# Kernel optimization log

Measured on AMD Instinct MI355X. Metric: run time of the kernel, lower is better.

The kernel has to match this reference:

```python
import jax, jax.numpy as jnp
import numpy as np

B, T, J, C, H = 16, 448, 448, 1024, 16
HD = C // H
NEG_INF = float('-inf')


def _layernorm(x, g, b, eps=1e-5):
    mu = jnp.mean(x, axis=-1, keepdims=True)
    var = jnp.var(x, axis=-1, keepdims=True)
    return (x - mu) * jax.lax.rsqrt(var + eps) * g + b


def _heads(x):
    # [B, S, C] -> [B, H, S, HD]
    Bv, S, _ = x.shape
    return x.reshape(Bv, S, H, HD).transpose(0, 2, 1, 3)


def _merge(x):
    # [B, H, S, HD] -> [B, S, C]
    Bv, _, S, _ = x.shape
    return x.transpose(0, 2, 1, 3).reshape(Bv, S, C)


def setup_inputs() -> dict:
    key = jax.random.key(0)
    ks = jax.random.split(key, 16)
    s = 0.02
    return {
        'tgt': jax.random.normal(ks[0], (B, T, C), jnp.float32),
        'src': jax.random.normal(ks[1], (B, J, C), jnp.float32),
        'sa_wqkv': jax.random.normal(ks[2], (C, 3 * C), jnp.float32) * s,
        'sa_wproj': jax.random.normal(ks[3], (C, C), jnp.float32) * s,
        'sa_bproj': jnp.zeros((C,), jnp.float32),
        'ed_wkv': jax.random.normal(ks[4], (C, 2 * C), jnp.float32) * s,
        'ed_wq': jax.random.normal(ks[5], (C, C), jnp.float32) * s,
        'ed_wproj': jax.random.normal(ks[6], (C, C), jnp.float32) * s,
        'ed_bproj': jnp.zeros((C,), jnp.float32),
        'ff_w1': jax.random.normal(ks[7], (C, 4 * C), jnp.float32) * s,
        'ff_b1': jnp.zeros((4 * C,), jnp.float32),
        'ff_w2': jax.random.normal(ks[8], (4 * C, C), jnp.float32) * s,
        'ff_b2': jnp.zeros((C,), jnp.float32),
        'ln1_g': jnp.ones((C,), jnp.float32), 'ln1_b': jnp.zeros((C,), jnp.float32),
        'ln2_g': jnp.ones((C,), jnp.float32), 'ln2_b': jnp.zeros((C,), jnp.float32),
        'ln3_g': jnp.ones((C,), jnp.float32), 'ln3_b': jnp.zeros((C,), jnp.float32),
        'tgt_padding_mask': jnp.zeros((B, T), bool),
    }


def _forward(tgt, src, sa_wqkv, sa_wproj, sa_bproj, ed_wkv, ed_wq, ed_wproj, ed_bproj,
             ff_w1, ff_b1, ff_w2, ff_b2, ln1_g, ln1_b, ln2_g, ln2_b, ln3_g, ln3_b,
             tgt_padding_mask):
    scale = C ** (-0.5)  # NOTE: original scales by full n_embd, not head_size

    # --- masked self-attention on ln1(tgt) ---
    x = _layernorm(tgt, ln1_g, ln1_b)
    qkv = x @ sa_wqkv
    q, k, v = (_heads(t) for t in jnp.split(qkv, 3, axis=-1))
    wei = jnp.einsum('bhtd,bhsd->bhts', q, k) * scale  # [B,H,T,T]
    causal = jnp.tril(jnp.ones((T, T), bool))
    wei = jnp.where(causal[None, None], wei, NEG_INF)
    wei = jnp.where(tgt_padding_mask[:, None, None, :], NEG_INF, wei)
    wei = jax.nn.softmax(wei, axis=-1)
    sa_out = _merge(jnp.einsum('bhts,bhsd->bhtd', wei, v)) @ sa_wproj + sa_bproj
    result = tgt + sa_out

    # --- cross-attention: ln2 applied to BOTH result and src (as in source) ---
    xq = _layernorm(result, ln2_g, ln2_b)
    xs = _layernorm(src, ln2_g, ln2_b)
    kv = xs @ ed_wkv
    k2, v2 = (_heads(t) for t in jnp.split(kv, 2, axis=-1))
    q2 = _heads(xq @ ed_wq)
    wei2 = jnp.einsum('bhtd,bhjd->bhtj', q2, k2) * scale  # [B,H,T,J]
    wei2 = jax.nn.softmax(wei2, axis=-1)
    ed_out = _merge(jnp.einsum('bhtj,bhjd->bhtd', wei2, v2)) @ ed_wproj + ed_bproj
    result = result + ed_out

    # --- FFN on ln3(tgt) (source uses tgt, not result) ---
    h = jax.nn.relu(_layernorm(tgt, ln3_g, ln3_b) @ ff_w1 + ff_b1)
    result = result + (h @ ff_w2 + ff_b2)
    return result


def reference(tgt, src, sa_wqkv, sa_wproj, sa_bproj, ed_wkv, ed_wq, ed_wproj, ed_bproj,
              ff_w1, ff_b1, ff_w2, ff_b2, ln1_g, ln1_b, ln2_g, ln2_b, ln3_g, ln3_b,
              tgt_padding_mask):
    return _forward(tgt, src, sa_wqkv, sa_wproj, sa_bproj, ed_wkv, ed_wq, ed_wproj,
                    ed_bproj, ff_w1, ff_b1, ff_w2, ff_b2, ln1_g, ln1_b, ln2_g, ln2_b,
                    ln3_g, ln3_b, tgt_padding_mask)
```

## Files before the change

kernel.cpp:

```cpp
#include <hip/hip_runtime.h>

typedef __bf16 bf16;
typedef __bf16 bf16x8 __attribute__((ext_vector_type(8)));
typedef float floatx4 __attribute__((ext_vector_type(4)));

__device__ __forceinline__ floatx4 mfma16(bf16x8 a, bf16x8 b, floatx4 c) {
    return __builtin_amdgcn_mfma_f32_16x16x32_bf16(a, b, c, 0, 0, 0);
}

__device__ __forceinline__ void load16_lds(const void* g, void* l) {
    __builtin_amdgcn_global_load_lds(
        (const __attribute__((address_space(1))) void*)g,
        (__attribute__((address_space(3))) void*)(unsigned int)(unsigned long long)l,
        16, 0, 0);
}

__global__ __launch_bounds__(256) void detect_dtype(const bf16* __restrict__ p,
                                                    int* __restrict__ flag) {
    __shared__ int bad;
    if (threadIdx.x == 0) bad = 0;
    __syncthreads();
    int lbad = 0;
    for (int i = threadIdx.x; i < 4096; i += 256) {
        const float v = (float)p[i];
        if (!isfinite(v) || fabsf(v) > 1e10f) lbad = 1;
    }
    if (lbad) atomicOr(&bad, 1);
    __syncthreads();
    if (threadIdx.x == 0) *flag = bad;
}

__global__ __launch_bounds__(256) void convert_vecs(
    const void* bpr, const void* bep, const void* fb1, const void* fb2,
    const void* g1, const void* b1, const void* g2, const void* b2,
    const void* g3, const void* b3, bf16* __restrict__ out,
    const int* __restrict__ flagp) {
    const int fl = *flagp;
    const int idx = blockIdx.x * 256 + threadIdx.x;
    const void* src;
    int off;
    if (idx < 1024)      { src = bpr; off = idx; }
    else if (idx < 2048) { src = bep; off = idx - 1024; }
    else if (idx < 6144) { src = fb1; off = idx - 2048; }
    else if (idx < 7168) { src = fb2; off = idx - 6144; }
    else {
        const void* t[6] = {g1, b1, g2, b2, g3, b3};
        src = t[(idx - 7168) >> 10];
        off = idx & 1023;
    }
    out[idx] = fl ? (bf16)((const float*)src)[off] : ((const bf16*)src)[off];
}

__global__ __launch_bounds__(256) void ln_f32(const float* __restrict__ X,
                                              const bf16* __restrict__ G,
                                              const bf16* __restrict__ Bv,
                                              bf16* __restrict__ Y) {
    const int row = blockIdx.x;
    const int tid = threadIdx.x;
    const float* x = X + (size_t)row * 1024 + tid * 4;
    float v[4];
#pragma unroll
    for (int i = 0; i < 4; i++) v[i] = x[i];
    float s = v[0] + v[1] + v[2] + v[3];
    float q = v[0] * v[0] + v[1] * v[1] + v[2] * v[2] + v[3] * v[3];
#pragma unroll
    for (int off = 32; off >= 1; off >>= 1) {
        s += __shfl_xor(s, off);
        q += __shfl_xor(q, off);
    }
    __shared__ float ss[4], qq[4];
    const int wave = tid >> 6, lane = tid & 63;
    if (lane == 0) { ss[wave] = s; qq[wave] = q; }
    __syncthreads();
    s = ss[0] + ss[1] + ss[2] + ss[3];
    q = qq[0] + qq[1] + qq[2] + qq[3];
    const float mu = s * (1.0f / 1024.0f);
    const float var = q * (1.0f / 1024.0f) - mu * mu;
    const float rs = rsqrtf(var + 1e-5f);
    bf16* y = Y + (size_t)row * 1024 + tid * 4;
    const bf16* g = G + tid * 4;
    const bf16* b = Bv + tid * 4;
#pragma unroll
    for (int i = 0; i < 4; i++)
        y[i] = (bf16)((v[i] - mu) * rs * (float)g[i] + (float)b[i]);
}

__global__ __launch_bounds__(256) void ln_dyn(const void* __restrict__ X,
                                              const bf16* __restrict__ G,
                                              const bf16* __restrict__ Bv,
                                              bf16* __restrict__ Y,
                                              const int* __restrict__ flagp) {
    const int fl = *flagp;
    const int row = blockIdx.x;
    const int tid = threadIdx.x;
    float v[4];
    if (fl) {
        const float* x = (const float*)X + (size_t)row * 1024 + tid * 4;
#pragma unroll
        for (int i = 0; i < 4; i++) v[i] = x[i];
    } else {
        const bf16* x = (const bf16*)X + (size_t)row * 1024 + tid * 4;
#pragma unroll
        for (int i = 0; i < 4; i++) v[i] = (float)x[i];
    }
    float s = v[0] + v[1] + v[2] + v[3];
    float q = v[0] * v[0] + v[1] * v[1] + v[2] * v[2] + v[3] * v[3];
#pragma unroll
    for (int off = 32; off >= 1; off >>= 1) {
        s += __shfl_xor(s, off);
        q += __shfl_xor(q, off);
    }
    __shared__ float ss[4], qq[4];
    const int wave = tid >> 6, lane = tid & 63;
    if (lane == 0) { ss[wave] = s; qq[wave] = q; }
    __syncthreads();
    s = ss[0] + ss[1] + ss[2] + ss[3];
    q = qq[0] + qq[1] + qq[2] + qq[3];
    const float mu = s * (1.0f / 1024.0f);
    const float var = q * (1.0f / 1024.0f) - mu * mu;
    const float rs = rsqrtf(var + 1e-5f);
    bf16* y = Y + (size_t)row * 1024 + tid * 4;
    const bf16* g = G + tid * 4;
    const bf16* b = Bv + tid * 4;
#pragma unroll
    for (int i = 0; i < 4; i++)
        y[i] = (bf16)((v[i] - mu) * rs * (float)g[i] + (float)b[i]);
}

__global__ __launch_bounds__(256) void transpose_all(
    const void* w0, const void* w1, const void* w2, const void* w3,
    const void* w4, const void* w5, const void* w6,
    bf16* __restrict__ out_base, const int* __restrict__ flagp) {
    const int fl = *flagp;
    const int cum[8] = {0, 3072, 4096, 6144, 7168, 8192, 12288, 16384};
    const int ntv[7] = {96, 32, 64, 32, 32, 128, 32};
    const int ldi[7] = {3072, 1024, 2048, 1024, 1024, 4096, 1024};
    const int ldo[7] = {1024, 1024, 1024, 1024, 1024, 1024, 4096};
    const size_t ooff[7] = {0, 3145728, 4194304, 6291456, 7340032, 8388608, 12582912};
    const void* ws[7] = {w0, w1, w2, w3, w4, w5, w6};

    const int g = blockIdx.x;
    int w = 0;
#pragma unroll
    for (int i = 1; i < 7; i++) if (g >= cum[i]) w = i;
    const int t = g - cum[w];
    const int xt = t % ntv[w], yt = t / ntv[w];
    const int n0 = xt * 32, k0 = yt * 32;
    const void* in = ws[w];
    bf16* out = out_base + ooff[w];
    const int ldin = ldi[w], ldout = ldo[w];

    __shared__ bf16 tile[32][33];
    const int x = threadIdx.x, y = threadIdx.y;
#pragma unroll
    for (int i = 0; i < 4; i++) {
        const size_t idx = (size_t)(k0 + y + 8 * i) * ldin + n0 + x;
        tile[y + 8 * i][x] = fl ? (bf16)((const float*)in)[idx]
                                : ((const bf16*)in)[idx];
    }
    __syncthreads();
#pragma unroll
    for (int i = 0; i < 4; i++)
        out[(size_t)(n0 + y + 8 * i) * ldout + k0 + x] = tile[x][y + 8 * i];
}

template <int TN>
__global__ __launch_bounds__(256) void gemm_bt(
    const bf16* __restrict__ A, int lda,
    const bf16* __restrict__ Bt, int ldb,
    const bf16* __restrict__ bias,
    const void* resd,
    const float* resf,
    bf16* outb, float* outf, void* dual,
    const int* __restrict__ flagp,
    int M, int N, int K, int relu) {
    constexpr int NJ = TN / 32;
    __shared__ bf16 As[128 * 64];
    __shared__ bf16 Bs[TN * 64];
    const int fl = *flagp;
    const int tid = threadIdx.x;
    const int wave = tid >> 6, lane = tid & 63;
    const int quad = lane >> 4, l16 = lane & 15;
    const int g = blockIdx.x;
    const int yb = g % 56, xb = g / 56;
    const int m0 = yb * 128, n0 = xb * TN;
    const int wm = (wave >> 1) * 64, wn = (wave & 1) * (TN / 2);

    const int srow = tid >> 3;
    const int sc = (tid & 7) ^ (srow & 7);
    const bf16* gA = A + (size_t)(m0 + srow) * lda + sc * 8;
    const bf16* gB = Bt + (size_t)(n0 + srow) * ldb + sc * 8;

    floatx4 acc[4][NJ] = {};

    for (int k0 = 0; k0 < K; k0 += 64) {
#pragma unroll
        for (int i = 0; i < 4; i++)
            load16_lds(gA + k0 + (size_t)(32 * i) * lda, &As[tid * 8 + i * 2048]);
#pragma unroll
        for (int i = 0; i < TN / 32; i++)
            load16_lds(gB + k0 + (size_t)(32 * i) * ldb, &Bs[tid * 8 + i * 2048]);
        __syncthreads();
        bf16x8 af[4][2], bfr[NJ][2];
#pragma unroll
        for (int i = 0; i < 4; i++)
#pragma unroll
            for (int h = 0; h < 2; h++) {
                const int r = wm + i * 16 + l16;
                const int slot = ((h << 2) + quad) ^ (r & 7);
                af[i][h] = *(const bf16x8*)(&As[r * 64 + slot * 8]);
            }
#pragma unroll
        for (int j = 0; j < NJ; j++)
#pragma unroll
            for (int h = 0; h < 2; h++) {
                const int r = wn + j * 16 + l16;
                const int slot = ((h << 2) + quad) ^ (r & 7);
                bfr[j][h] = *(const bf16x8*)(&Bs[r * 64 + slot * 8]);
            }
#pragma unroll
        for (int i = 0; i < 4; i++)
#pragma unroll
            for (int j = 0; j < NJ; j++) {
                acc[i][j] = mfma16(af[i][0], bfr[j][0], acc[i][j]);
                acc[i][j] = mfma16(af[i][1], bfr[j][1], acc[i][j]);
            }
        __syncthreads();
    }

#pragma unroll
    for (int i = 0; i < 4; i++) {
        const int mbase = m0 + wm + i * 16 + quad * 4;
#pragma unroll
        for (int j = 0; j < NJ; j++) {
            const int n = n0 + wn + j * 16 + l16;
            const float bv = bias ? (float)bias[n] : 0.0f;
#pragma unroll
            for (int r = 0; r < 4; r++) {
                const size_t idx = (size_t)(mbase + r) * N + n;
                float v = acc[i][j][r] + bv;
                if (relu && v < 0.0f) v = 0.0f;
                if (resd) v += fl ? ((const float*)resd)[idx]
                                  : (float)((const bf16*)resd)[idx];
                if (resf) v += resf[idx];
                if (dual) {
                    if (fl) ((float*)dual)[idx] = v;
                    else ((bf16*)dual)[idx] = (bf16)v;
                } else if (outf) {
                    outf[idx] = v;
                } else {
                    outb[idx] = (bf16)v;
                }
            }
        }
    }
}

__global__ __launch_bounds__(256) void attn_kernel(
    const bf16* __restrict__ Q, int qstride,
    const bf16* __restrict__ Kp, int kstride,
    const bf16* __restrict__ Vp, int vstride,
    bf16* __restrict__ O, int causal) {
    const int T_ = 448, HD = 64, OC = 1024;
    const float scale = 0.03125f;
    const int bh = blockIdx.y, b = bh >> 4, h = bh & 15;
    const int q0 = blockIdx.x * 32;
    const int tid = threadIdx.x, wave = tid >> 6, lane = tid & 63;
    const int quad = lane >> 4, l16 = lane & 15;

    __shared__ bf16 Pb[32][464];
    __shared__ bf16 VT[64][40];
    __shared__ float redp[32][4];
    __shared__ float Mbuf[32], Lbuf[32];

    const bf16* qb = Q + (size_t)(b * T_ + q0) * qstride + h * HD;
    const bf16* kb = Kp + (size_t)(b * T_) * kstride + h * HD;
    const bf16* vb = Vp + (size_t)(b * T_) * vstride + h * HD;

    bf16x8 qf[2][2];
#pragma unroll
    for (int qi = 0; qi < 2; qi++)
#pragma unroll
        for (int kh = 0; kh < 2; kh++)
            qf[qi][kh] = *(const bf16x8*)(qb + (size_t)(qi * 16 + l16) * qstride + kh * 32 + quad * 8);

    float S[2][7][4];
#pragma unroll
    for (int kt = 0; kt < 7; kt++) {
        const int s = wave * 112 + kt * 16 + l16;
        const bf16* kr = kb + (size_t)s * kstride + quad * 8;
        bf16x8 kf0 = *(const bf16x8*)kr;
        bf16x8 kf1 = *(const bf16x8*)(kr + 32);
#pragma unroll
        for (int qi = 0; qi < 2; qi++) {
            floatx4 c = {};
            c = mfma16(qf[qi][0], kf0, c);
            c = mfma16(qf[qi][1], kf1, c);
#pragma unroll
            for (int r = 0; r < 4; r++) {
                float v = c[r] * scale;
                if (causal) {
                    const int t = q0 + qi * 16 + quad * 4 + r;
                    if (s > t) v = -30000.0f;
                }
                S[qi][kt][r] = v;
            }
        }
    }

    float mx[2][4];
#pragma unroll
    for (int qi = 0; qi < 2; qi++)
#pragma unroll
        for (int r = 0; r < 4; r++) {
            float m = S[qi][0][r];
#pragma unroll
            for (int kt = 1; kt < 7; kt++) m = fmaxf(m, S[qi][kt][r]);
#pragma unroll
            for (int off = 1; off < 16; off <<= 1) m = fmaxf(m, __shfl_xor(m, off));
            mx[qi][r] = m;
        }
    if (l16 == 0) {
#pragma unroll
        for (int qi = 0; qi < 2; qi++)
#pragma unroll
            for (int r = 0; r < 4; r++) redp[qi * 16 + quad * 4 + r][wave] = mx[qi][r];
    }
    __syncthreads();
    if (tid < 32)
        Mbuf[tid] = fmaxf(fmaxf(redp[tid][0], redp[tid][1]),
                          fmaxf(redp[tid][2], redp[tid][3]));
    __syncthreads();

#pragma unroll
    for (int qi = 0; qi < 2; qi++)
#pragma unroll
        for (int r = 0; r < 4; r++) {
            const float Mv = Mbuf[qi * 16 + quad * 4 + r];
            float acc = 0.0f;
#pragma unroll
            for (int kt = 0; kt < 7; kt++) {
                const float p = __expf(fminf(S[qi][kt][r] - Mv, 0.0f));
                acc += p;
                Pb[qi * 16 + quad * 4 + r][wave * 112 + kt * 16 + l16] = (bf16)p;
            }
#pragma unroll
            for (int off = 1; off < 16; off <<= 1) acc += __shfl_xor(acc, off);
            if (l16 == 0) redp[qi * 16 + quad * 4 + r][wave] = acc;
        }
    __syncthreads();
    if (tid < 32)
        Lbuf[tid] = redp[tid][0] + redp[tid][1] + redp[tid][2] + redp[tid][3];

    floatx4 oacc[2] = {};
    const int qi3 = wave & 1, djb = (wave >> 1) * 2;
    for (int kt = 0; kt < 14; kt++) {
        const int s0 = kt * 32;
        const bf16* vsrc = vb + (size_t)(s0 + (tid & 31)) * vstride + (tid >> 5) * 8;
        bf16x8 vv = *(const bf16x8*)vsrc;
        __syncthreads();
#pragma unroll
        for (int e = 0; e < 8; e++) VT[(tid >> 5) * 8 + e][tid & 31] = vv[e];
        __syncthreads();
        bf16x8 pa = *(const bf16x8*)(&Pb[qi3 * 16 + l16][s0 + quad * 8]);
#pragma unroll
        for (int u = 0; u < 2; u++) {
            bf16x8 bv = *(const bf16x8*)(&VT[(djb + u) * 16 + l16][quad * 8]);
            oacc[u] = mfma16(pa, bv, oacc[u]);
        }
    }

#pragma unroll
    for (int u = 0; u < 2; u++) {
        const int d = (djb + u) * 16 + l16;
#pragma unroll
        for (int r = 0; r < 4; r++) {
            const int t = q0 + qi3 * 16 + quad * 4 + r;
            const float L = Lbuf[qi3 * 16 + quad * 4 + r];
            O[(size_t)(b * T_ + t) * OC + h * HD + d] = (bf16)(oacc[u][r] / L);
        }
    }
}

extern "C" void kernel_launch(void* const* d_in, const int* in_sizes, int n_in,
                              void* d_out, int out_size, void* d_ws, size_t ws_size,
                              hipStream_t stream) {
    const void* tgt_r  = d_in[0];
    const void* src_r  = d_in[1];
    const void* wqkv_r = d_in[2];
    const void* wpr_r  = d_in[3];
    const void* bpr_r  = d_in[4];
    const void* wkv_r  = d_in[5];
    const void* wq_r   = d_in[6];
    const void* wep_r  = d_in[7];
    const void* bep_r  = d_in[8];
    const void* fw1_r  = d_in[9];
    const void* fb1_r  = d_in[10];
    const void* fw2_r  = d_in[11];
    const void* fb2_r  = d_in[12];
    const void* l1g_r  = d_in[13];
    const void* l1b_r  = d_in[14];
    const void* l2g_r  = d_in[15];
    const void* l2b_r  = d_in[16];
    const void* l3g_r  = d_in[17];
    const void* l3b_r  = d_in[18];

    const size_t MB = 1u << 20;
    char* base = (char*)d_ws;
    bf16*  WT   = (bf16*)(base + 0 * MB);
    float* resf = (float*)(base + 32 * MB);
    bf16*  Cb   = (bf16*)(base + 60 * MB);
    bf16*  Hb   = Cb;
    bf16*  Db   = (bf16*)(base + 102 * MB);
    bf16*  x3b  = (bf16*)(base + 116 * MB);
    bf16*  vecs = (bf16*)(base + 130 * MB);
    int*   flag = (int*)(base + 130 * MB + 65536);
    bf16*  kvb  = Cb + (size_t)7168 * 1024;

    bf16* T_qkv = WT + 0;
    bf16* T_pr  = WT + 3145728;
    bf16* T_kv  = WT + 4194304;
    bf16* T_q   = WT + 6291456;
    bf16* T_ep  = WT + 7340032;
    bf16* T_f1  = WT + 8388608;
    bf16* T_f2  = WT + 12582912;

    bf16* v_bpr = vecs + 0;
    bf16* v_bep = vecs + 1024;
    bf16* v_fb1 = vecs + 2048;
    bf16* v_fb2 = vecs + 6144;
    bf16 *v_l1g = vecs + 7168,  *v_l1b = vecs + 8192;
    bf16 *v_l2g = vecs + 9216,  *v_l2b = vecs + 10240;
    bf16 *v_l3g = vecs + 11264, *v_l3b = vecs + 12288;

    const int M = 7168;
    dim3 blk(256);
    dim3 tb(32, 8);

    detect_dtype<<<1, blk, 0, stream>>>((const bf16*)tgt_r, flag);
    convert_vecs<<<52, blk, 0, stream>>>(bpr_r, bep_r, fb1_r, fb2_r, l1g_r, l1b_r,
                                         l2g_r, l2b_r, l3g_r, l3b_r, vecs, flag);
    transpose_all<<<16384, tb, 0, stream>>>(wqkv_r, wpr_r, wkv_r, wq_r, wep_r,
                                            fw1_r, fw2_r, WT, flag);

    ln_dyn<<<M, blk, 0, stream>>>(tgt_r, v_l1g, v_l1b, Db, flag);
    gemm_bt<128><<<24 * 56, blk, 0, stream>>>(
        Db, 1024, T_qkv, 1024, nullptr, nullptr, nullptr, Cb, nullptr, nullptr,
        flag, M, 3072, 1024, 0);
    attn_kernel<<<dim3(14, 256), blk, 0, stream>>>(Cb, 3072, Cb + 1024, 3072, Cb + 2048, 3072, Db, 1);
    gemm_bt<64><<<16 * 56, blk, 0, stream>>>(
        Db, 1024, T_pr, 1024, v_bpr, tgt_r, nullptr, nullptr, resf, nullptr,
        flag, M, 1024, 1024, 0);
    ln_f32<<<M, blk, 0, stream>>>(resf, v_l2g, v_l2b, Db);
    ln_dyn<<<M, blk, 0, stream>>>(src_r, v_l2g, v_l2b, Cb, flag);
    gemm_bt<128><<<16 * 56, blk, 0, stream>>>(
        Cb, 1024, T_kv, 1024, nullptr, nullptr, nullptr, kvb, nullptr, nullptr,
        flag, M, 2048, 1024, 0);
    gemm_bt<64><<<16 * 56, blk, 0, stream>>>(
        Db, 1024, T_q, 1024, nullptr, nullptr, nullptr, Cb, nullptr, nullptr,
        flag, M, 1024, 1024, 0);
    attn_kernel<<<dim3(14, 256), blk, 0, stream>>>(Cb, 1024, kvb, 2048, kvb + 1024, 2048, Db, 0);
    gemm_bt<64><<<16 * 56, blk, 0, stream>>>(
        Db, 1024, T_ep, 1024, v_bep, nullptr, resf, nullptr, resf, nullptr,
        flag, M, 1024, 1024, 0);
    ln_dyn<<<M, blk, 0, stream>>>(tgt_r, v_l3g, v_l3b, x3b, flag);
    gemm_bt<128><<<32 * 56, blk, 0, stream>>>(
        x3b, 1024, T_f1, 1024, v_fb1, nullptr, nullptr, Hb, nullptr, nullptr,
        flag, M, 4096, 1024, 1);
    gemm_bt<64><<<16 * 56, blk, 0, stream>>>(
        Hb, 4096, T_f2, 4096, v_fb2, nullptr, resf, nullptr, nullptr, d_out,
        flag, M, 1024, 4096, 0);
}
```

Measured before the change: 624.8 us.

## Double-buffer GEMM LDS tiles with prefetch of next-next k-tile

The GEMM main loop now keeps two LDS buffers for the A and B tiles. It prefetches tile t+2 via global_load_lds while MFMAs run on the current tile, and uses manual vmcnt/lgkmcnt waits and raw barriers to order the stages. This is meant to overlap global-memory latency with compute instead of stalling on a full sync every k-step. In exchange it doubles LDS usage, which may reduce occupancy, and it relies on hand-counted vmcnt values.

```diff
diff --git a/kernel.cpp b/kernel.cpp
--- a/kernel.cpp
+++ b/kernel.cpp
@@ -14,6 +14,11 @@
         (__attribute__((address_space(3))) void*)(unsigned int)(unsigned long long)l,
         16, 0, 0);
 }
+
+#define PIPE_BARRIER do { asm volatile("" ::: "memory"); \
+    __builtin_amdgcn_s_barrier(); asm volatile("" ::: "memory"); } while (0)
+#define PIPE_LGKM0 do { asm volatile("s_waitcnt lgkmcnt(0)" ::: "memory"); \
+    __builtin_amdgcn_sched_barrier(0); } while (0)
 
 __global__ __launch_bounds__(256) void detect_dtype(const bf16* __restrict__ p,
                                                     int* __restrict__ flag) {
@@ -175,8 +180,9 @@
     const int* __restrict__ flagp,
     int M, int N, int K, int relu) {
     constexpr int NJ = TN / 32;
-    __shared__ bf16 As[128 * 64];
-    __shared__ bf16 Bs[TN * 64];
+    constexpr int NB = TN / 32;
+    __shared__ bf16 As[2][128 * 64];
+    __shared__ bf16 Bs[2][TN * 64];
     const int fl = *flagp;
     const int tid = threadIdx.x;
     const int wave = tid >> 6, lane = tid & 63;
@@ -191,16 +197,31 @@
     const bf16* gA = A + (size_t)(m0 + srow) * lda + sc * 8;
     const bf16* gB = Bt + (size_t)(n0 + srow) * ldb + sc * 8;
 
+    const int NT = K >> 6;
+
+#define STAGE_TILE(T) do { \
+    const int _b = (T) & 1; \
+    const int _k = (T) << 6; \
+    _Pragma("unroll") \
+    for (int i = 0; i < 4; i++) \
+        load16_lds(gA + _k + (size_t)(32 * i) * lda, \
+                   &As[_b][tid * 8 + i * 2048]); \
+    _Pragma("unroll") \
+    for (int i = 0; i < NB; i++) \
+        load16_lds(gB + _k + (size_t)(32 * i) * ldb, \
+                   &Bs[_b][tid * 8 + i * 2048]); \
+} while (0)
+
     floatx4 acc[4][NJ] = {};
 
-    for (int k0 = 0; k0 < K; k0 += 64) {
-#pragma unroll
-        for (int i = 0; i < 4; i++)
-            load16_lds(gA + k0 + (size_t)(32 * i) * lda, &As[tid * 8 + i * 2048]);
-#pragma unroll
-        for (int i = 0; i < TN / 32; i++)
-            load16_lds(gB + k0 + (size_t)(32 * i) * ldb, &Bs[tid * 8 + i * 2048]);
-        __syncthreads();
+    STAGE_TILE(0);
+    STAGE_TILE(1);
+    if constexpr (TN == 128) asm volatile("s_waitcnt vmcnt(8)" ::: "memory");
+    else                     asm volatile("s_waitcnt vmcnt(6)" ::: "memory");
+    PIPE_BARRIER;
+
+    for (int t = 0; t < NT; ++t) {
+        const int cur = t & 1;
         bf16x8 af[4][2], bfr[NJ][2];
 #pragma unroll
         for (int i = 0; i < 4; i++)
@@ -208,7 +229,7 @@
             for (int h = 0; h < 2; h++) {
                 const int r = wm + i * 16 + l16;
                 const int slot = ((h << 2) + quad) ^ (r & 7);
-                af[i][h] = *(const bf16x8*)(&As[r * 64 + slot * 8]);
+                af[i][h] = *(const bf16x8*)(&As[cur][r * 64 + slot * 8]);
             }
 #pragma unroll
         for (int j = 0; j < NJ; j++)
@@ -216,8 +237,11 @@
             for (int h = 0; h < 2; h++) {
                 const int r = wn + j * 16 + l16;
                 const int slot = ((h << 2) + quad) ^ (r & 7);
-                bfr[j][h] = *(const bf16x8*)(&Bs[r * 64 + slot * 8]);
+                bfr[j][h] = *(const bf16x8*)(&Bs[cur][r * 64 + slot * 8]);
             }
+        PIPE_LGKM0;
+        PIPE_BARRIER;
+        if (t + 2 < NT) STAGE_TILE(t + 2);
 #pragma unroll
         for (int i = 0; i < 4; i++)
 #pragma unroll
@@ -225,8 +249,15 @@
                 acc[i][j] = mfma16(af[i][0], bfr[j][0], acc[i][j]);
                 acc[i][j] = mfma16(af[i][1], bfr[j][1], acc[i][j]);
             }
-        __syncthreads();
-    }
+        if (t + 2 < NT) {
+            if constexpr (TN == 128) asm volatile("s_waitcnt vmcnt(8)" ::: "memory");
+            else                     asm volatile("s_waitcnt vmcnt(6)" ::: "memory");
+        } else {
+            asm volatile("s_waitcnt vmcnt(0)" ::: "memory");
+        }
+        PIPE_BARRIER;
+    }
+#undef STAGE_TILE
 
 #pragma unroll
     for (int i = 0; i < 4; i++) {
```

After: 593.4 us. 1.05x faster.
